# Kernel tuning notes

Measured on AMD Instinct MI355X. Metric: run time of the kernel, lower is better.

The kernel has to match this reference:

```python
import jax, jax.numpy as jnp
import numpy as np

V, C, DFF, NH, NL, KS, OUT = 256, 192, 768, 2, 6, 3, 192
B, T, W = 64, 512, 4
DH = C // NH
PAD = KS // 2
DN = ('NCH', 'OIH', 'NCH')


def _rel_to_abs(x):
    # [b,h,l,2l-1] -> [b,h,l,l]  (VITS _relative_position_to_absolute_position)
    b, h, l, _ = x.shape
    x = jnp.pad(x, ((0, 0), (0, 0), (0, 0), (0, 1)))
    x = x.reshape(b, h, l * 2 * l)
    x = jnp.pad(x, ((0, 0), (0, 0), (0, l - 1)))
    x = x.reshape(b, h, l + 1, 2 * l - 1)
    return x[:, :, :l, l - 1:]


def _abs_to_rel(x):
    # [b,h,l,l] -> [b,h,l,2l-1]  (VITS _absolute_position_to_relative_position)
    b, h, l, _ = x.shape
    x = jnp.pad(x, ((0, 0), (0, 0), (0, 0), (0, l - 1)))
    x = x.reshape(b, h, l * (2 * l - 1))
    x = jnp.pad(x, ((0, 0), (0, 0), (l, 0)))
    x = x.reshape(b, h, l, 2 * l)
    return x[:, :, :, 1:]


def _get_rel_emb(emb, length):
    # emb: [2W+1, DH] -> [2*length-1, DH]
    pad_len = max(length - (W + 1), 0)
    start = max(W + 1 - length, 0)
    padded = jnp.pad(emb, ((pad_len, pad_len), (0, 0)))
    return padded[start:start + 2 * length - 1]


def _ln(x, g, b):
    mu = jnp.mean(x, -1, keepdims=True)
    var = jnp.mean(jnp.square(x - mu), -1, keepdims=True)
    return (x - mu) * jax.lax.rsqrt(var + 1e-5) * g + b


def setup_inputs():
    key = jax.random.key(0)
    ks = jax.random.split(key, 12)
    n = lambda k, s, std: jax.random.normal(k, s, jnp.float32) * std
    return dict(
        tokens=jax.random.randint(ks[0], (B, T), 0, V),
        x_lengths=jnp.full((B,), T, dtype=jnp.int32),
        emb_w=n(ks[1], (V, C), C ** -0.5),
        wqkv=n(ks[2], (NL, 3, C, C), 0.02),
        bqkv=jnp.zeros((NL, 3, C), jnp.float32),
        wo=n(ks[3], (NL, C, C), 0.02),
        bo=jnp.zeros((NL, C), jnp.float32),
        rel_k=n(ks[4], (NL, 2 * W + 1, DH), DH ** -0.5),
        rel_v=n(ks[5], (NL, 2 * W + 1, DH), DH ** -0.5),
        ln1_g=jnp.ones((NL, C), jnp.float32),
        ln1_b=jnp.zeros((NL, C), jnp.float32),
        ln2_g=jnp.ones((NL, C), jnp.float32),
        ln2_b=jnp.zeros((NL, C), jnp.float32),
        ffn_w1=n(ks[6], (NL, DFF, C, KS), 0.02),
        ffn_b1=jnp.zeros((NL, DFF), jnp.float32),
        ffn_w2=n(ks[7], (NL, C, DFF, KS), 0.02),
        ffn_b2=jnp.zeros((NL, C), jnp.float32),
        proj_w=n(ks[8], (2 * OUT, C), 0.02),
        proj_b=jnp.zeros((2 * OUT,), jnp.float32),
    )


def reference(tokens, x_lengths, emb_w, wqkv, bqkv, wo, bo, rel_k, rel_v,
              ln1_g, ln1_b, ln2_g, ln2_b, ffn_w1, ffn_b1, ffn_w2, ffn_b2,
              proj_w, proj_b):
    x = emb_w[tokens] * (C ** 0.5)                       # [B,T,C]
    mask = (jnp.arange(T)[None, :] < x_lengths[:, None]).astype(x.dtype)  # [B,T]
    bias = jnp.where((mask[:, None, :, None] * mask[:, None, None, :]) > 0.0, 0.0, -1e4)
    x = x * mask[..., None]
    inv_sqrt_d = DH ** -0.5
    for l in range(NL):
        q = jnp.einsum('btc,oc->bto', x, wqkv[l, 0]) + bqkv[l, 0]
        k = jnp.einsum('btc,oc->bto', x, wqkv[l, 1]) + bqkv[l, 1]
        v = jnp.einsum('btc,oc->bto', x, wqkv[l, 2]) + bqkv[l, 2]
        q = q.reshape(B, T, NH, DH).transpose(0, 2, 1, 3)  # [B,H,T,D]
        k = k.reshape(B, T, NH, DH).transpose(0, 2, 1, 3)
        v = v.reshape(B, T, NH, DH).transpose(0, 2, 1, 3)
        scores = jnp.einsum('bhtd,bhsd->bhts', q, k) * inv_sqrt_d
        rk = _get_rel_emb(rel_k[l], T)                     # [2T-1, D]
        rel_logits = jnp.einsum('bhtd,md->bhtm', q * inv_sqrt_d, rk)
        scores = scores + _rel_to_abs(rel_logits)
        p = jax.nn.softmax(scores + bias, axis=-1)
        o = jnp.einsum('bhts,bhsd->bhtd', p, v)
        o = o + jnp.einsum('bhtm,md->bhtd', _abs_to_rel(p), _get_rel_emb(rel_v[l], T))
        o = o.transpose(0, 2, 1, 3).reshape(B, T, C)
        y = jnp.einsum('btc,oc->bto', o, wo[l]) + bo[l]
        x = _ln(x + y, ln1_g[l], ln1_b[l])
        h = jax.lax.conv_general_dilated((x * mask[..., None]).transpose(0, 2, 1),
                                         ffn_w1[l], (1,), [(PAD, PAD)],
                                         dimension_numbers=DN) + ffn_b1[l][None, :, None]
        h = jax.nn.relu(h) * mask[:, None, :]
        h = jax.lax.conv_general_dilated(h, ffn_w2[l], (1,), [(PAD, PAD)],
                                         dimension_numbers=DN) + ffn_b2[l][None, :, None]
        y = h.transpose(0, 2, 1) * mask[..., None]
        x = _ln(x + y, ln2_g[l], ln2_b[l])
    x = x * mask[..., None]
    stats = (jnp.einsum('btc,oc->bto', x, proj_w) + proj_b) * mask[..., None]
    m, logs = jnp.split(stats, 2, axis=-1)
    x_mask = mask[:, None, :]
    return x.transpose(0, 2, 1), m.transpose(0, 2, 1), logs.transpose(0, 2, 1), x_mask
```

## Files before the change

### kernel.cpp

```cpp
#include <hip/hip_runtime.h>
#include <hip/hip_bf16.h>

typedef __hip_bfloat16 bf16;
typedef __attribute__((ext_vector_type(8))) short short8;
typedef __attribute__((ext_vector_type(4))) float f32x4;

#define NB 64
#define NT 512
#define NC 192
#define NHEAD 2
#define NDH 96
#define NLAYER 6
#define NDFF 768
#define NW 4

constexpr int MROWS = NB * NT;
constexpr size_t MC = (size_t)MROWS * NC;
constexpr size_t MCB = MC * 4;

__device__ __forceinline__ float us2f(unsigned short x) { return __uint_as_float((unsigned)x << 16); }
__device__ __forceinline__ unsigned short f2b(float f) {
    bf16 h = __float2bfloat16(f);
    return *reinterpret_cast<unsigned short*>(&h);
}

__global__ __launch_bounds__(256) void cvt_plain(const float* __restrict__ s, bf16* __restrict__ d, int n) {
    int i = blockIdx.x * 256 + threadIdx.x;
    if (i < n) d[i] = __float2bfloat16(s[i]);
}
__global__ __launch_bounds__(256) void cvt_conv(const float* __restrict__ s, bf16* __restrict__ d,
                                                int L, int N, int C) {
    int i = blockIdx.x * 256 + threadIdx.x;
    if (i >= L * N * C * 3) return;
    int dk = i % 3;
    int rest = i / 3;
    int c = rest % C;
    int rest2 = rest / C;
    int n = rest2 % N;
    int l = rest2 / N;
    d[(((size_t)l * 3 + dk) * N + n) * C + c] = __float2bfloat16(s[i]);
}

__global__ __launch_bounds__(256) void embed_kernel(const int* __restrict__ tok,
                                                    const int* __restrict__ lens,
                                                    const float* __restrict__ emb,
                                                    float* __restrict__ x,
                                                    bf16* __restrict__ xb) {
    int idx = blockIdx.x * 256 + threadIdx.x;
    if (idx >= (int)MC) return;
    int c = idx % NC;
    int m = idx / NC;
    int t = m % NT, b = m / NT;
    float v = emb[tok[m] * NC + c] * 13.856406460551018f;
    if (t >= lens[b]) v = 0.f;
    x[idx] = v;
    xb[idx] = __float2bfloat16(v);
}

enum GMode { GM_QKV = 0, GM_CONV1 = 2, GM_PROJ = 4 };

template <int MODE, int NTOT, int KC, int TAPS>
__global__ __launch_bounds__(256) void gemm_mfma(const bf16* __restrict__ A,
                                                 const bf16* __restrict__ W,
                                                 const float* __restrict__ bias,
                                                 const int* __restrict__ lens,
                                                 float* __restrict__ of,
                                                 bf16* __restrict__ ob1,
                                                 bf16* __restrict__ ob2,
                                                 bf16* __restrict__ ob3) {
    constexpr int RA = (TAPS == 3) ? 130 : 128;
    constexpr int RB = TAPS * 64;
    __shared__ unsigned short As[RA * 40];
    __shared__ unsigned short Bs[RB * 40];
    const int tid = threadIdx.x;
    const int w = tid >> 6, lane = tid & 63;
    const int g = lane >> 4, li = lane & 15;
    const int n0 = blockIdx.x * 64;
    const int m0 = blockIdx.y * 128;
    const int b = m0 >> 9, t0 = m0 & 511;
    const int len = lens[b];
    const unsigned short* Au = (const unsigned short*)A;
    const unsigned short* Wu = (const unsigned short*)W;

    f32x4 acc[2][4];
#pragma unroll
    for (int a = 0; a < 2; a++)
#pragma unroll
        for (int s = 0; s < 4; s++) acc[a][s] = (f32x4){0.f, 0.f, 0.f, 0.f};

#pragma unroll 1
    for (int k0 = 0; k0 < KC; k0 += 32) {
        __syncthreads();
        for (int c = tid; c < RA * 2; c += 256) {
            int i = c >> 1, hf = (c & 1) * 16;
            int t = t0 + i - (TAPS == 3 ? 1 : 0);
            bool valid = (t >= 0) && (t < NT);
            if constexpr (MODE == GM_CONV1) valid = valid && (t < len);
            short8 v0{}, v1{};
            if (valid) {
                const unsigned short* src = Au + ((size_t)(b * NT + t) * KC + k0 + hf);
                v0 = *(const short8*)src;
                v1 = *(const short8*)(src + 8);
            }
            *(short8*)&As[i * 40 + hf] = v0;
            *(short8*)&As[i * 40 + hf + 8] = v1;
        }
        for (int c = tid; c < RB * 4; c += 256) {
            int rb = c >> 2, qq = (c & 3) * 8;
            int dk = rb >> 6, nl = rb & 63;
            *(short8*)&Bs[rb * 40 + qq] =
                *(const short8*)(Wu + ((size_t)(dk * NTOT + n0 + nl) * KC + k0 + qq));
        }
        __syncthreads();
#pragma unroll
        for (int dk = 0; dk < TAPS; dk++) {
            short8 af0 = *(const short8*)&As[(w * 32 + li + dk) * 40 + g * 8];
            short8 af1 = *(const short8*)&As[(w * 32 + 16 + li + dk) * 40 + g * 8];
#pragma unroll
            for (int sub = 0; sub < 4; sub++) {
                short8 bfr = *(const short8*)&Bs[(dk * 64 + sub * 16 + li) * 40 + g * 8];
                acc[0][sub] = __builtin_amdgcn_mfma_f32_16x16x32_bf16(af0, bfr, acc[0][sub], 0, 0, 0);
                acc[1][sub] = __builtin_amdgcn_mfma_f32_16x16x32_bf16(af1, bfr, acc[1][sub], 0, 0, 0);
            }
        }
    }

#pragma unroll
    for (int sub = 0; sub < 4; sub++) {
        int n = n0 + sub * 16 + li;
        float bv = bias[n];
#pragma unroll
        for (int a = 0; a < 2; a++) {
#pragma unroll
            for (int rr = 0; rr < 4; rr++) {
                int t = t0 + w * 32 + a * 16 + g * 4 + rr;
                size_t m = (size_t)(b * NT + t);
                float vv = acc[a][sub][rr] + bv;
                if constexpr (MODE == GM_QKV) {
                    int iw = n / NC;
                    int cc = n - iw * NC;
                    int hh = cc >= NDH ? 1 : 0;
                    int d = cc - hh * NDH;
                    int bh = b * NHEAD + hh;
                    if (iw == 0) ob1[((size_t)bh * NT + t) * NDH + d] = __float2bfloat16(vv);
                    else if (iw == 1) ob2[((size_t)bh * NT + t) * NDH + d] = __float2bfloat16(vv);
                    else ob3[((size_t)bh * NDH + d) * NT + t] = __float2bfloat16(vv);
                } else if constexpr (MODE == GM_CONV1) {
                    vv = vv > 0.f ? vv : 0.f;
                    if (t >= len) vv = 0.f;
                    ob1[m * NDFF + n] = __float2bfloat16(vv);
                } else {
                    if (t >= len) vv = 0.f;
                    int half = n >= 192 ? 1 : 0;
                    int cc = n - half * 192;
                    of[(size_t)(half + 1) * MC + ((size_t)b * NC + cc) * NT + t] = vv;
                }
            }
        }
    }
}

template <int KC, int TAPS, bool MASKY>
__global__ __launch_bounds__(512) void gemm_ln(const bf16* __restrict__ A,
                                               const bf16* __restrict__ W,
                                               const float* __restrict__ bias,
                                               const int* __restrict__ lens,
                                               const float* __restrict__ lng,
                                               const float* __restrict__ lnb,
                                               float* __restrict__ x,
                                               bf16* __restrict__ xb) {
    constexpr int RA = (TAPS == 3) ? 130 : 128;
    constexpr int RB = TAPS * 192;
    constexpr int NSTEP = KC / 32;
    constexpr int NBI = (RB * 4 + 511) / 512;
    __shared__ unsigned short As[RA * 40];
    __shared__ unsigned short Bs[RB * 40];
    __shared__ float rsm[128][4];
    __shared__ float rsq[128][4];
    const int tid = threadIdx.x;
    const int lane = tid & 63;
    const int g = lane >> 4, li = lane & 15;
    const int w = tid >> 6;
    const int wr = w & 1, wc = w >> 1;
    const int m0 = blockIdx.x * 128;
    const int b = m0 >> 9, t0 = m0 & 511;
    const int len = lens[b];
    const unsigned short* Au = (const unsigned short*)A;
    const unsigned short* Wu = (const unsigned short*)W;

    const int ai = tid >> 1, ahf = (tid & 1) * 16;
    const int at = t0 + ai - (TAPS == 3 ? 1 : 0);
    const bool aon = (tid < RA * 2);
    const bool avalid = aon && (at >= 0) && (at < NT);

    short8 ra0{}, ra1{};
    short8 rbv[NBI];
#pragma unroll
    for (int j = 0; j < NBI; j++) rbv[j] = short8{};

    f32x4 acc[4][3];
#pragma unroll
    for (int ar = 0; ar < 4; ar++)
#pragma unroll
        for (int sub = 0; sub < 3; sub++) acc[ar][sub] = (f32x4){0.f, 0.f, 0.f, 0.f};

    if (avalid) {
        const unsigned short* src = Au + ((size_t)(b * NT + at) * KC + 0 + ahf);
        ra0 = *(const short8*)src;
        ra1 = *(const short8*)(src + 8);
    }
#pragma unroll
    for (int j = 0; j < NBI; j++) {
        int cb = tid + j * 512;
        if (cb < RB * 4) {
            int rbr = cb >> 2, qq = (cb & 3) * 8;
            rbv[j] = *(const short8*)(Wu + ((size_t)rbr * KC + 0 + qq));
        }
    }
    if (aon) {
        short8 z{};
        *(short8*)&As[ai * 40 + ahf] = avalid ? ra0 : z;
        *(short8*)&As[ai * 40 + ahf + 8] = avalid ? ra1 : z;
    }
#pragma unroll
    for (int j = 0; j < NBI; j++) {
        int cb = tid + j * 512;
        if (cb < RB * 4) {
            int rbr = cb >> 2, qq = (cb & 3) * 8;
            *(short8*)&Bs[rbr * 40 + qq] = rbv[j];
        }
    }

#pragma unroll 1
    for (int s = 0; s < NSTEP; s++) {
        __syncthreads();
        if (s + 1 < NSTEP) {
            int k0 = (s + 1) * 32;
            if (avalid) {
                const unsigned short* src = Au + ((size_t)(b * NT + at) * KC + k0 + ahf);
                ra0 = *(const short8*)src;
                ra1 = *(const short8*)(src + 8);
            }
#pragma unroll
            for (int j = 0; j < NBI; j++) {
                int cb = tid + j * 512;
                if (cb < RB * 4) {
                    int rbr = cb >> 2, qq = (cb & 3) * 8;
                    rbv[j] = *(const short8*)(Wu + ((size_t)rbr * KC + k0 + qq));
                }
            }
        }
#pragma unroll
        for (int dk = 0; dk < TAPS; dk++) {
            short8 af[4];
#pragma unroll
            for (int ar = 0; ar < 4; ar++)
                af[ar] = *(const short8*)&As[(wr * 64 + ar * 16 + li + dk) * 40 + g * 8];
#pragma unroll
            for (int sub = 0; sub < 3; sub++) {
                short8 bfr = *(const short8*)&Bs[(dk * 192 + wc * 48 + sub * 16 + li) * 40 + g * 8];
#pragma unroll
                for (int ar = 0; ar < 4; ar++)
                    acc[ar][sub] = __builtin_amdgcn_mfma_f32_16x16x32_bf16(af[ar], bfr, acc[ar][sub], 0, 0, 0);
            }
        }
        __syncthreads();
        if (s + 1 < NSTEP) {
            if (aon) {
                short8 z{};
                *(short8*)&As[ai * 40 + ahf] = avalid ? ra0 : z;
                *(short8*)&As[ai * 40 + ahf + 8] = avalid ? ra1 : z;
            }
#pragma unroll
            for (int j = 0; j < NBI; j++) {
                int cb = tid + j * 512;
                if (cb < RB * 4) {
                    int rbr = cb >> 2, qq = (cb & 3) * 8;
                    *(short8*)&Bs[rbr * 40 + qq] = rbv[j];
                }
            }
        }
    }

    float biasv[3], gv[3], bbv[3];
#pragma unroll
    for (int sub = 0; sub < 3; sub++) {
        int n = wc * 48 + sub * 16 + li;
        biasv[sub] = bias[n];
        gv[sub] = lng[n];
        bbv[sub] = lnb[n];
    }
    float psm[4][4], psq[4][4];
#pragma unroll
    for (int ar = 0; ar < 4; ar++) {
#pragma unroll
        for (int rr = 0; rr < 4; rr++) {
            int r = wr * 64 + ar * 16 + 4 * g + rr;
            int t = t0 + r;
            size_t m = (size_t)(b * NT + t);
            float sm = 0.f, sq = 0.f;
#pragma unroll
            for (int sub = 0; sub < 3; sub++) {
                int n = wc * 48 + sub * 16 + li;
                float y = acc[ar][sub][rr] + biasv[sub];
                if (MASKY && t >= len) y = 0.f;
                float rres = y + x[m * NC + n];
                acc[ar][sub][rr] = rres;
                sm += rres;
                sq += rres * rres;
            }
            psm[ar][rr] = sm;
            psq[ar][rr] = sq;
        }
    }
#pragma unroll
    for (int off = 1; off < 16; off <<= 1) {
#pragma unroll
        for (int ar = 0; ar < 4; ar++)
#pragma unroll
            for (int rr = 0; rr < 4; rr++) {
                psm[ar][rr] += __shfl_xor(psm[ar][rr], off);
                psq[ar][rr] += __shfl_xor(psq[ar][rr], off);
            }
    }
    if (li == 0) {
#pragma unroll
        for (int ar = 0; ar < 4; ar++)
#pragma unroll
            for (int rr = 0; rr < 4; rr++) {
                int r = wr * 64 + ar * 16 + 4 * g + rr;
                rsm[r][wc] = psm[ar][rr];
                rsq[r][wc] = psq[ar][rr];
            }
    }
    __syncthreads();
#pragma unroll
    for (int ar = 0; ar < 4; ar++) {
#pragma unroll
        for (int rr = 0; rr < 4; rr++) {
            int r = wr * 64 + ar * 16 + 4 * g + rr;
            int t = t0 + r;
            size_t m = (size_t)(b * NT + t);
            float sm = rsm[r][0] + rsm[r][1] + rsm[r][2] + rsm[r][3];
            float sq = rsq[r][0] + rsq[r][1] + rsq[r][2] + rsq[r][3];
            float mu = sm * (1.f / NC);
            float var = fmaxf(sq * (1.f / NC) - mu * mu, 0.f);
            float rs = rsqrtf(var + 1e-5f);
#pragma unroll
            for (int sub = 0; sub < 3; sub++) {
                int n = wc * 48 + sub * 16 + li;
                float o = (acc[ar][sub][rr] - mu) * rs * gv[sub] + bbv[sub];
                x[m * NC + n] = o;
                xb[m * NC + n] = __float2bfloat16(o);
            }
        }
    }
}

__global__ __launch_bounds__(256, 4) void attn_mfma(const bf16* __restrict__ q,
                                                    const bf16* __restrict__ k,
                                                    const bf16* __restrict__ v,
                                                    const float* __restrict__ relk,
                                                    const float* __restrict__ relv,
                                                    const int* __restrict__ lens,
                                                    bf16* __restrict__ o) {
    __shared__ __align__(16) char pool[40448];
    unsigned short* Kt = (unsigned short*)pool;
    unsigned short* Vt = (unsigned short*)(pool + 13312);
    unsigned short* Pt = (unsigned short*)(pool + 27136);
    unsigned short* Pb = (unsigned short*)(pool + 36352);
    unsigned short* Qt = (unsigned short*)pool;
    unsigned short* Rk = (unsigned short*)(pool + 13312);

    const int qt = blockIdx.x, bh = blockIdx.y;
    const int b = bh >> 1, h = bh & 1;
    const int q0 = qt * 64;
    const int tid = threadIdx.x;
    const int w = tid >> 6, lane = tid & 63;
    const int g = lane >> 4, li = lane & 15;
    const int len = lens[b];
    const float scale = 0.10206207261596575f;

    const unsigned short* qg = (const unsigned short*)q + (size_t)bh * NT * NDH;
    const unsigned short* kg = (const unsigned short*)k + (size_t)bh * NT * NDH;
    const unsigned short* vg = (const unsigned short*)v + (size_t)bh * NDH * NT;

    for (int c = tid; c < 64 * 12; c += 256) {
        int r = c / 12, seg = (c % 12) * 8;
        *(short8*)&Qt[r * 104 + seg] = *(const short8*)(qg + (size_t)(q0 + r) * NDH + seg);
    }
    for (int c = tid; c < 16 * 96; c += 256) {
        int dd = c / 96, d = c - (c / 96) * 96;
        Rk[dd * 104 + d] = (dd < 9) ? f2b(relk[dd * 96 + d]) : (unsigned short)0;
    }
    for (int c = tid; c < 4 * 16 * 32; c += 256) Pb[c] = 0;
    __syncthreads();

    f32x4 racc = (f32x4){0.f, 0.f, 0.f, 0.f};
    short8 qf[3];
#pragma unroll
    for (int kk = 0; kk < 3; kk++) {
        qf[kk] = *(const short8*)&Qt[(w * 16 + li) * 104 + kk * 32 + g * 8];
        short8 bfr = *(const short8*)&Rk[li * 104 + kk * 32 + g * 8];
        racc = __builtin_amdgcn_mfma_f32_16x16x32_bf16(qf[kk], bfr, racc, 0, 0, 0);
    }
    short8 rvf[6];
#pragma unroll
    for (int ds = 0; ds < 6; ds++) {
#pragma unroll
        for (int i = 0; i < 8; i++) {
            int j = g * 8 + i;
            int d = ds * 16 + li;
            unsigned short u = (j < 9) ? f2b(relv[j * 96 + d]) : (unsigned short)0;
            rvf[ds][i] = (short)u;
        }
    }
    __syncthreads();

    float m_run[4], l_run[4];
    f32x4 Oa[6];
#pragma unroll
    for (int rr = 0; rr < 4; rr++) { m_run[rr] = -1e30f; l_run[rr] = 0.f; }
#pragma unroll
    for (int ds = 0; ds < 6; ds++) Oa[ds] = (f32x4){0.f, 0.f, 0.f, 0.f};

    for (int s0 = 0; s0 < NT; s0 += 64) {
        for (int c = tid; c < 64 * 12; c += 256) {
            int ss = c / 12, seg = (c % 12) * 8;
            *(short8*)&Kt[ss * 104 + seg] = *(const short8*)(kg + (size_t)(s0 + ss) * NDH + seg);
        }
        for (int c = tid; c < 96 * 8; c += 256) {
            int d = c >> 3, seg = (c & 7) * 8;
            *(short8*)&Vt[d * 72 + seg] = *(const short8*)(vg + (size_t)d * NT + s0 + seg);
        }
        __syncthreads();

        f32x4 acc[4];
#pragma unroll
        for (int sub = 0; sub < 4; sub++) acc[sub] = (f32x4){0.f, 0.f, 0.f, 0.f};
        __builtin_amdgcn_s_setprio(1);
#pragma unroll
        for (int kk = 0; kk < 3; kk++) {
#pragma unroll
            for (int sub = 0; sub < 4; sub++) {
                short8 bfr = *(const short8*)&Kt[(sub * 16 + li) * 104 + kk * 32 + g * 8];
                acc[sub] = __builtin_amdgcn_mfma_f32_16x16x32_bf16(qf[kk], bfr, acc[sub], 0, 0, 0);
            }
        }
        __builtin_amdgcn_s_setprio(0);

        float rmax[4];
#pragma unroll
        for (int rr = 0; rr < 4; rr++) rmax[rr] = -1e30f;
#pragma unroll
        for (int sub = 0; sub < 4; sub++) {
#pragma unroll
            for (int rr = 0; rr < 4; rr++) {
                int scol = s0 + sub * 16 + li;
                int rloc = w * 16 + 4 * g + rr;
                int qrow = q0 + rloc;
                int dd = scol - qrow;
                float rv = __shfl(racc[rr], g * 16 + dd + NW);
                float val = acc[sub][rr];
                if (dd >= -NW && dd <= NW) val += rv;
                val *= scale;
                if (scol >= len || qrow >= len) val -= 10000.f;
                acc[sub][rr] = val;
                rmax[rr] = fmaxf(rmax[rr], val);
            }
        }
#pragma unroll
        for (int off = 1; off < 16; off <<= 1)
#pragma unroll
            for (int rr = 0; rr < 4; rr++) rmax[rr] = fmaxf(rmax[rr], __shfl_xor(rmax[rr], off));

        float scf[4];
#pragma unroll
        for (int rr = 0; rr < 4; rr++) {
            float mn = fmaxf(m_run[rr], rmax[rr]);
            scf[rr] = __expf(m_run[rr] - mn);
            m_run[rr] = mn;
        }
        float rsum[4] = {0.f, 0.f, 0.f, 0.f};
#pragma unroll
        for (int sub = 0; sub < 4; sub++)
#pragma unroll
            for (int rr = 0; rr < 4; rr++) {
                float p = __expf(acc[sub][rr] - m_run[rr]);
                acc[sub][rr] = p;
                rsum[rr] += p;
            }
#pragma unroll
        for (int off = 1; off < 16; off <<= 1)
#pragma unroll
            for (int rr = 0; rr < 4; rr++) rsum[rr] += __shfl_xor(rsum[rr], off);
#pragma unroll
        for (int rr = 0; rr < 4; rr++) l_run[rr] = l_run[rr] * scf[rr] + rsum[rr];
#pragma unroll
        for (int ds = 0; ds < 6; ds++)
#pragma unroll
            for (int rr = 0; rr < 4; rr++) Oa[ds][rr] *= scf[rr];

#pragma unroll
        for (int sub = 0; sub < 4; sub++)
#pragma unroll
            for (int rr = 0; rr < 4; rr++)
                Pt[w * 1152 + (4 * g + rr) * 72 + sub * 16 + li] = f2b(acc[sub][rr]);

        __builtin_amdgcn_s_setprio(1);
#pragma unroll
        for (int kk = 0; kk < 2; kk++) {
            short8 pa = *(const short8*)&Pt[w * 1152 + li * 72 + kk * 32 + g * 8];
#pragma unroll
            for (int ds = 0; ds < 6; ds++) {
                short8 bv = *(const short8*)&Vt[(ds * 16 + li) * 72 + kk * 32 + g * 8];
                Oa[ds] = __builtin_amdgcn_mfma_f32_16x16x32_bf16(pa, bv, Oa[ds], 0, 0, 0);
            }
        }
        __builtin_amdgcn_s_setprio(0);

        for (int c = lane; c < 144; c += 64) {
            int r = c / 9, j = c - (c / 9) * 9;
            int s = q0 + w * 16 + r + j - NW;
            unsigned short pv_ = 0;
            int u = s - s0;
            if (u >= 0 && u < 64) pv_ = Pt[w * 1152 + r * 72 + u];
            Pb[w * 512 + r * 32 + j] = pv_;
        }
        short8 pband = *(const short8*)&Pb[w * 512 + li * 32 + g * 8];
#pragma unroll
        for (int ds = 0; ds < 6; ds++)
            Oa[ds] = __builtin_amdgcn_mfma_f32_16x16x32_bf16(pband, rvf[ds], Oa[ds], 0, 0, 0);
        __syncthreads();
    }

    float invl[4];
#pragma unroll
    for (int rr = 0; rr < 4; rr++) invl[rr] = 1.f / l_run[rr];
#pragma unroll
    for (int ds = 0; ds < 6; ds++)
#pragma unroll
        for (int rr = 0; rr < 4; rr++) {
            int qrow = q0 + w * 16 + 4 * g + rr;
            o[((size_t)(b * NT + qrow)) * NC + h * 96 + ds * 16 + li] =
                __float2bfloat16(Oa[ds][rr] * invl[rr]);
        }
}

__global__ __launch_bounds__(256) void xpose_kernel(const float* __restrict__ x,
                                                    const int* __restrict__ lens,
                                                    float* __restrict__ out) {
    int idx = blockIdx.x * 256 + threadIdx.x;
    if (idx >= (int)MC) return;
    int t = idx % NT;
    int bc = idx / NT;
    int c = bc % NC;
    int b = bc / NC;
    float v = (t < lens[b]) ? x[((size_t)b * NT + t) * NC + c] : 0.f;
    out[idx] = v;
}

__global__ __launch_bounds__(256) void mask_kernel(const int* __restrict__ lens, float* __restrict__ out) {
    int idx = blockIdx.x * 256 + threadIdx.x;
    if (idx >= NB * NT) return;
    int t = idx % NT;
    int b = idx / NT;
    out[idx] = (t < lens[b]) ? 1.f : 0.f;
}

extern "C" void kernel_launch(void* const* d_in, const int* in_sizes, int n_in,
                              void* d_out, int out_size, void* d_ws, size_t ws_size,
                              hipStream_t stream) {
    (void)in_sizes; (void)n_in; (void)out_size; (void)ws_size;
    const int* tok = (const int*)d_in[0];
    const int* lens = (const int*)d_in[1];
    const float* emb = (const float*)d_in[2];
    const float* wqkv = (const float*)d_in[3];
    const float* bqkv = (const float*)d_in[4];
    const float* wo = (const float*)d_in[5];
    const float* bo = (const float*)d_in[6];
    const float* relk = (const float*)d_in[7];
    const float* relv = (const float*)d_in[8];
    const float* ln1g = (const float*)d_in[9];
    const float* ln1b = (const float*)d_in[10];
    const float* ln2g = (const float*)d_in[11];
    const float* ln2b = (const float*)d_in[12];
    const float* fw1 = (const float*)d_in[13];
    const float* fb1 = (const float*)d_in[14];
    const float* fw2 = (const float*)d_in[15];
    const float* fb2 = (const float*)d_in[16];
    const float* pw = (const float*)d_in[17];
    const float* pb = (const float*)d_in[18];
    float* out = (float*)d_out;

    char* wsb = (char*)d_ws;
    float* xB = (float*)wsb;
    bf16* xb = (bf16*)(wsb + 2 * MCB);
    bf16* qb = (bf16*)(wsb + 2 * MCB + MCB / 2);
    bf16* kb = qb + MC;
    bf16* vb = kb + MC;
    bf16* ob = vb + MC;
    bf16* hB = qb;
    bf16* pwqkv = ob + MC;
    bf16* pwo = pwqkv + (size_t)NLAYER * 3 * NC * NC;
    bf16* pw1 = pwo + (size_t)NLAYER * NC * NC;
    bf16* pw2 = pw1 + (size_t)NLAYER * 3 * NDFF * NC;
    bf16* pproj = pw2 + (size_t)NLAYER * 3 * NC * NDFF;

    {
        int n1 = NLAYER * 3 * NC * NC;
        cvt_plain<<<(n1 + 255) / 256, 256, 0, stream>>>(wqkv, pwqkv, n1);
        int n2 = NLAYER * NC * NC;
        cvt_plain<<<(n2 + 255) / 256, 256, 0, stream>>>(wo, pwo, n2);
        int n3 = 2 * 192 * NC;
        cvt_plain<<<(n3 + 255) / 256, 256, 0, stream>>>(pw, pproj, n3);
        int n4 = NLAYER * NDFF * NC * 3;
        cvt_conv<<<(n4 + 255) / 256, 256, 0, stream>>>(fw1, pw1, NLAYER, NDFF, NC);
        int n5 = NLAYER * NC * NDFF * 3;
        cvt_conv<<<(n5 + 255) / 256, 256, 0, stream>>>(fw2, pw2, NLAYER, NC, NDFF);
    }

    embed_kernel<<<(int)((MC + 255) / 256), 256, 0, stream>>>(tok, lens, emb, xB, xb);

    for (int l = 0; l < NLAYER; l++) {
        gemm_mfma<GM_QKV, 576, 192, 1><<<dim3(9, 256), 256, 0, stream>>>(
            xb, pwqkv + (size_t)l * 3 * NC * NC, bqkv + (size_t)l * 3 * NC, lens,
            nullptr, qb, kb, vb);
        attn_mfma<<<dim3(8, NB * NHEAD), 256, 0, stream>>>(
            qb, kb, vb, relk + (size_t)l * (2 * NW + 1) * NDH,
            relv + (size_t)l * (2 * NW + 1) * NDH, lens, ob);
        gemm_ln<192, 1, false><<<256, 512, 0, stream>>>(
            ob, pwo + (size_t)l * NC * NC, bo + (size_t)l * NC, lens,
            ln1g + (size_t)l * NC, ln1b + (size_t)l * NC, xB, xb);
        gemm_mfma<GM_CONV1, 768, 192, 3><<<dim3(12, 256), 256, 0, stream>>>(
            xb, pw1 + (size_t)l * 3 * NDFF * NC, fb1 + (size_t)l * NDFF, lens,
            nullptr, hB, nullptr, nullptr);
        gemm_ln<768, 3, true><<<256, 512, 0, stream>>>(
            hB, pw2 + (size_t)l * 3 * NC * NDFF, fb2 + (size_t)l * NC, lens,
            ln2g + (size_t)l * NC, ln2b + (size_t)l * NC, xB, xb);
    }

    gemm_mfma<GM_PROJ, 384, 192, 1><<<dim3(6, 256), 256, 0, stream>>>(
        xb, pproj, pb, lens, out, nullptr, nullptr, nullptr);
    xpose_kernel<<<(int)((MC + 255) / 256), 256, 0, stream>>>(xB, lens, out);
    mask_kernel<<<(NB * NT + 255) / 256, 256, 0, stream>>>(lens, out + 3 * MC);
}
```

Baseline: 1.539 ms.

## Add dedicated pipelined conv1 GEMM and streamline attention softmax with exp2 and lazy rescale

Replaces the generic three-tap conv1 GEMM path with a new 512-thread kernel. It uses 128x192 tiles, register-prefetched double staging, and 4x3 MFMA tiles per wave, giving more reuse per LDS load. Attention now takes Q pre-scaled by softmax scale·log2e in the QKV epilogue, uses exp2f, and skips the mask check when the sequence is full. It also rescales the running max only when it grows past a threshold, and swaps grid dimensions so heads vary fastest. The lazy rescale trades exactness of the running max for fewer multiplies, and the larger conv tile uses more LDS and registers.

After: 1.558 ms. Within noise of the previous version (+1.2%).

```diff
diff --git a/kernel.cpp b/kernel.cpp
--- a/kernel.cpp
+++ b/kernel.cpp
@@ -17,6 +17,7 @@
 constexpr int MROWS = NB * NT;
 constexpr size_t MC = (size_t)MROWS * NC;
 constexpr size_t MCB = MC * 4;
+constexpr float QSC = 0.10206207261596575f * 1.4426950408889634f;
 
 __device__ __forceinline__ float us2f(unsigned short x) { return __uint_as_float((unsigned)x << 16); }
 __device__ __forceinline__ unsigned short f2b(float f) {
@@ -57,9 +58,9 @@
     xb[idx] = __float2bfloat16(v);
 }
 
-enum GMode { GM_QKV = 0, GM_CONV1 = 2, GM_PROJ = 4 };
-
-template <int MODE, int NTOT, int KC, int TAPS>
+enum GMode { GM_QKV = 0, GM_PROJ = 4 };
+
+template <int MODE, int NTOT, int KC>
 __global__ __launch_bounds__(256) void gemm_mfma(const bf16* __restrict__ A,
                                                  const bf16* __restrict__ W,
                                                  const float* __restrict__ bias,
@@ -68,8 +69,8 @@
                                                  bf16* __restrict__ ob1,
                                                  bf16* __restrict__ ob2,
                                                  bf16* __restrict__ ob3) {
-    constexpr int RA = (TAPS == 3) ? 130 : 128;
-    constexpr int RB = TAPS * 64;
+    constexpr int RA = 128;
+    constexpr int RB = 64;
     __shared__ unsigned short As[RA * 40];
     __shared__ unsigned short Bs[RB * 40];
     const int tid = threadIdx.x;
@@ -93,35 +94,24 @@
         __syncthreads();
         for (int c = tid; c < RA * 2; c += 256) {
             int i = c >> 1, hf = (c & 1) * 16;
-            int t = t0 + i - (TAPS == 3 ? 1 : 0);
-            bool valid = (t >= 0) && (t < NT);
-            if constexpr (MODE == GM_CONV1) valid = valid && (t < len);
-            short8 v0{}, v1{};
-            if (valid) {
-                const unsigned short* src = Au + ((size_t)(b * NT + t) * KC + k0 + hf);
-                v0 = *(const short8*)src;
-                v1 = *(const short8*)(src + 8);
-            }
-            *(short8*)&As[i * 40 + hf] = v0;
-            *(short8*)&As[i * 40 + hf + 8] = v1;
+            int t = t0 + i;
+            const unsigned short* src = Au + ((size_t)(b * NT + t) * KC + k0 + hf);
+            *(short8*)&As[i * 40 + hf] = *(const short8*)src;
+            *(short8*)&As[i * 40 + hf + 8] = *(const short8*)(src + 8);
         }
         for (int c = tid; c < RB * 4; c += 256) {
             int rb = c >> 2, qq = (c & 3) * 8;
-            int dk = rb >> 6, nl = rb & 63;
             *(short8*)&Bs[rb * 40 + qq] =
-                *(const short8*)(Wu + ((size_t)(dk * NTOT + n0 + nl) * KC + k0 + qq));
+                *(const short8*)(Wu + ((size_t)(n0 + rb) * KC + k0 + qq));
         }
         __syncthreads();
-#pragma unroll
-        for (int dk = 0; dk < TAPS; dk++) {
-            short8 af0 = *(const short8*)&As[(w * 32 + li + dk) * 40 + g * 8];
-            short8 af1 = *(const short8*)&As[(w * 32 + 16 + li + dk) * 40 + g * 8];
-#pragma unroll
-            for (int sub = 0; sub < 4; sub++) {
-                short8 bfr = *(const short8*)&Bs[(dk * 64 + sub * 16 + li) * 40 + g * 8];
-                acc[0][sub] = __builtin_amdgcn_mfma_f32_16x16x32_bf16(af0, bfr, acc[0][sub], 0, 0, 0);
-                acc[1][sub] = __builtin_amdgcn_mfma_f32_16x16x32_bf16(af1, bfr, acc[1][sub], 0, 0, 0);
-            }
+        short8 af0 = *(const short8*)&As[(w * 32 + li) * 40 + g * 8];
+        short8 af1 = *(const short8*)&As[(w * 32 + 16 + li) * 40 + g * 8];
+#pragma unroll
+        for (int sub = 0; sub < 4; sub++) {
+            short8 bfr = *(const short8*)&Bs[(sub * 16 + li) * 40 + g * 8];
+            acc[0][sub] = __builtin_amdgcn_mfma_f32_16x16x32_bf16(af0, bfr, acc[0][sub], 0, 0, 0);
+            acc[1][sub] = __builtin_amdgcn_mfma_f32_16x16x32_bf16(af1, bfr, acc[1][sub], 0, 0, 0);
         }
     }
 
@@ -142,19 +132,158 @@
                     int hh = cc >= NDH ? 1 : 0;
                     int d = cc - hh * NDH;
                     int bh = b * NHEAD + hh;
-                    if (iw == 0) ob1[((size_t)bh * NT + t) * NDH + d] = __float2bfloat16(vv);
+                    if (iw == 0) ob1[((size_t)bh * NT + t) * NDH + d] = __float2bfloat16(vv * QSC);
                     else if (iw == 1) ob2[((size_t)bh * NT + t) * NDH + d] = __float2bfloat16(vv);
                     else ob3[((size_t)bh * NDH + d) * NT + t] = __float2bfloat16(vv);
-                } else if constexpr (MODE == GM_CONV1) {
-                    vv = vv > 0.f ? vv : 0.f;
-                    if (t >= len) vv = 0.f;
-                    ob1[m * NDFF + n] = __float2bfloat16(vv);
                 } else {
                     if (t >= len) vv = 0.f;
                     int half = n >= 192 ? 1 : 0;
                     int cc = n - half * 192;
                     of[(size_t)(half + 1) * MC + ((size_t)b * NC + cc) * NT + t] = vv;
                 }
+            }
+        }
+    }
+}
+
+__global__ __launch_bounds__(512) void gemm_relu(const bf16* __restrict__ A,
+                                                 const bf16* __restrict__ W,
+                                                 const float* __restrict__ bias,
+                                                 const int* __restrict__ lens,
+                                                 bf16* __restrict__ ob) {
+    constexpr int KC = 192;
+    constexpr int RA = 130;
+    constexpr int RB = 576;
+    constexpr int NSTEP = KC / 32;
+    constexpr int NBI = (RB * 4 + 511) / 512;
+    __shared__ unsigned short As[RA * 40];
+    __shared__ unsigned short Bs[RB * 40];
+    const int tid = threadIdx.x;
+    const int lane = tid & 63;
+    const int g = lane >> 4, li = lane & 15;
+    const int w = tid >> 6;
+    const int wr = w & 1, wc = w >> 1;
+    const int m0 = blockIdx.x * 128;
+    const int n0 = blockIdx.y * 192;
+    const int b = m0 >> 9, t0 = m0 & 511;
+    const int len = lens[b];
+    const unsigned short* Au = (const unsigned short*)A;
+    const unsigned short* Wu = (const unsigned short*)W;
+
+    const int ai = tid >> 1, ahf = (tid & 1) * 16;
+    const int at = t0 + ai - 1;
+    const bool aon = (tid < RA * 2);
+    const bool avalid = aon && (at >= 0) && (at < NT) && (at < len);
+
+    short8 ra0{}, ra1{};
+    short8 rbv[NBI];
+#pragma unroll
+    for (int j = 0; j < NBI; j++) rbv[j] = short8{};
+
+    f32x4 acc[4][3];
+#pragma unroll
+    for (int ar = 0; ar < 4; ar++)
+#pragma unroll
+        for (int sub = 0; sub < 3; sub++) acc[ar][sub] = (f32x4){0.f, 0.f, 0.f, 0.f};
+
+    auto wrow = [&](int rb) -> size_t {
+        int dk = (rb >= 384) ? 2 : ((rb >= 192) ? 1 : 0);
+        int nl = rb - dk * 192;
+        return (size_t)(dk * NDFF + n0 + nl);
+    };
+
+    if (avalid) {
+        const unsigned short* src = Au + ((size_t)(b * NT + at) * KC + ahf);
+        ra0 = *(const short8*)src;
+        ra1 = *(const short8*)(src + 8);
+    }
+#pragma unroll
+    for (int j = 0; j < NBI; j++) {
+        int cb = tid + j * 512;
+        if (cb < RB * 4) {
+            int rbr = cb >> 2, qq = (cb & 3) * 8;
+            rbv[j] = *(const short8*)(Wu + (wrow(rbr) * KC + qq));
+        }
+    }
+    if (aon) {
+        short8 z{};
+        *(short8*)&As[ai * 40 + ahf] = avalid ? ra0 : z;
+        *(short8*)&As[ai * 40 + ahf + 8] = avalid ? ra1 : z;
+    }
+#pragma unroll
+    for (int j = 0; j < NBI; j++) {
+        int cb = tid + j * 512;
+        if (cb < RB * 4) {
+            int rbr = cb >> 2, qq = (cb & 3) * 8;
+            *(short8*)&Bs[rbr * 40 + qq] = rbv[j];
+        }
+    }
+
+#pragma unroll 1
+    for (int s = 0; s < NSTEP; s++) {
+        __syncthreads();
+        if (s + 1 < NSTEP) {
+            int k0 = (s + 1) * 32;
+            if (avalid) {
+                const unsigned short* src = Au + ((size_t)(b * NT + at) * KC + k0 + ahf);
+                ra0 = *(const short8*)src;
+                ra1 = *(const short8*)(src + 8);
+            }
+#pragma unroll
+            for (int j = 0; j < NBI; j++) {
+                int cb = tid + j * 512;
+                if (cb < RB * 4) {
+                    int rbr = cb >> 2, qq = (cb & 3) * 8;
+                    rbv[j] = *(const short8*)(Wu + (wrow(rbr) * KC + k0 + qq));
+                }
+            }
+        }
+#pragma unroll
+        for (int dk = 0; dk < 3; dk++) {
+            short8 af[4];
+#pragma unroll
+            for (int ar = 0; ar < 4; ar++)
+                af[ar] = *(const short8*)&As[(wr * 64 + ar * 16 + li + dk) * 40 + g * 8];
+#pragma unroll
+            for (int sub = 0; sub < 3; sub++) {
+                short8 bfr = *(const short8*)&Bs[(dk * 192 + wc * 48 + sub * 16 + li) * 40 + g * 8];
+#pragma unroll
+                for (int ar = 0; ar < 4; ar++)
+                    acc[ar][sub] = __builtin_amdgcn_mfma_f32_16x16x32_bf16(af[ar], bfr, acc[ar][sub], 0, 0, 0);
+            }
+        }
+        __syncthreads();
+        if (s + 1 < NSTEP) {
+            if (aon) {
+                short8 z{};
+                *(short8*)&As[ai * 40 + ahf] = avalid ? ra0 : z;
+                *(short8*)&As[ai * 40 + ahf + 8] = avalid ? ra1 : z;
+            }
+#pragma unroll
+            for (int j = 0; j < NBI; j++) {
+                int cb = tid + j * 512;
+                if (cb < RB * 4) {
+                    int rbr = cb >> 2, qq = (cb & 3) * 8;
+                    *(short8*)&Bs[rbr * 40 + qq] = rbv[j];
+                }
+            }
+        }
+    }
+
+#pragma unroll
+    for (int sub = 0; sub < 3; sub++) {
+        int n = n0 + wc * 48 + sub * 16 + li;
+        float bv = bias[n];
+#pragma unroll
+        for (int ar = 0; ar < 4; ar++) {
+#pragma unroll
+            for (int rr = 0; rr < 4; rr++) {
+                int t = t0 + wr * 64 + ar * 16 + 4 * g + rr;
+                size_t m = (size_t)(b * NT + t);
+                float vv = acc[ar][sub][rr] + bv;
+                vv = vv > 0.f ? vv : 0.f;
+                if (t >= len) vv = 0.f;
+                ob[m * NDFF + n] = __float2bfloat16(vv);
             }
         }
     }
@@ -372,14 +501,14 @@
     unsigned short* Qt = (unsigned short*)pool;
     unsigned short* Rk = (unsigned short*)(pool + 13312);
 
-    const int qt = blockIdx.x, bh = blockIdx.y;
+    const int bh = blockIdx.x, qt = blockIdx.y;
     const int b = bh >> 1, h = bh & 1;
     const int q0 = qt * 64;
     const int tid = threadIdx.x;
     const int w = tid >> 6, lane = tid & 63;
     const int g = lane >> 4, li = lane & 15;
     const int len = lens[b];
-    const float scale = 0.10206207261596575f;
+    const bool anymask = (len < NT);
 
     const unsigned short* qg = (const unsigned short*)q + (size_t)bh * NT * NDH;
     const unsigned short* kg = (const unsigned short*)k + (size_t)bh * NT * NDH;
@@ -457,14 +586,12 @@
 #pragma unroll
             for (int rr = 0; rr < 4; rr++) {
                 int scol = s0 + sub * 16 + li;
-                int rloc = w * 16 + 4 * g + rr;
-                int qrow = q0 + rloc;
+                int qrow = q0 + w * 16 + 4 * g + rr;
                 int dd = scol - qrow;
                 float rv = __shfl(racc[rr], g * 16 + dd + NW);
                 float val = acc[sub][rr];
                 if (dd >= -NW && dd <= NW) val += rv;
-                val *= scale;
-                if (scol >= len || qrow >= len) val -= 10000.f;
+                if (anymask && (scol >= len || qrow >= len)) val -= 14427.0f;
                 acc[sub][rr] = val;
                 rmax[rr] = fmaxf(rmax[rr], val);
             }
@@ -474,19 +601,26 @@
 #pragma unroll
             for (int rr = 0; rr < 4; rr++) rmax[rr] = fmaxf(rmax[rr], __shfl_xor(rmax[rr], off));
 
-        float scf[4];
-#pragma unroll
-        for (int rr = 0; rr < 4; rr++) {
-            float mn = fmaxf(m_run[rr], rmax[rr]);
-            scf[rr] = __expf(m_run[rr] - mn);
-            m_run[rr] = mn;
+        float growth = -3.0e38f;
+#pragma unroll
+        for (int rr = 0; rr < 4; rr++) growth = fmaxf(growth, rmax[rr] - m_run[rr]);
+        if (__any(growth > 11.54f)) {
+#pragma unroll
+            for (int rr = 0; rr < 4; rr++) {
+                float mn = fmaxf(m_run[rr], rmax[rr]);
+                float scf = exp2f(m_run[rr] - mn);
+                m_run[rr] = mn;
+                l_run[rr] *= scf;
+#pragma unroll
+                for (int ds = 0; ds < 6; ds++) Oa[ds][rr] *= scf;
+            }
         }
         float rsum[4] = {0.f, 0.f, 0.f, 0.f};
 #pragma unroll
         for (int sub = 0; sub < 4; sub++)
 #pragma unroll
             for (int rr = 0; rr < 4; rr++) {
-                float p = __expf(acc[sub][rr] - m_run[rr]);
+                float p = exp2f(acc[sub][rr] - m_run[rr]);
                 acc[sub][rr] = p;
                 rsum[rr] += p;
             }
@@ -495,11 +629,7 @@
 #pragma unroll
             for (int rr = 0; rr < 4; rr++) rsum[rr] += __shfl_xor(rsum[rr], off);
 #pragma unroll
-        for (int rr = 0; rr < 4; rr++) l_run[rr] = l_run[rr] * scf[rr] + rsum[rr];
-#pragma unroll
-        for (int ds = 0; ds < 6; ds++)
-#pragma unroll
-            for (int rr = 0; rr < 4; rr++) Oa[ds][rr] *= scf[rr];
+        for (int rr = 0; rr < 4; rr++) l_run[rr] += rsum[rr];
 
 #pragma unroll
         for (int sub = 0; sub < 4; sub++)
@@ -623,24 +753,23 @@
     embed_kernel<<<(int)((MC + 255) / 256), 256, 0, stream>>>(tok, lens, emb, xB, xb);
 
     for (int l = 0; l < NLAYER; l++) {
-        gemm_mfma<GM_QKV, 576, 192, 1><<<dim3(9, 256), 256, 0, stream>>>(
+        gemm_mfma<GM_QKV, 576, 192><<<dim3(9, 256), 256, 0, stream>>>(
             xb, pwqkv + (size_t)l * 3 * NC * NC, bqkv + (size_t)l * 3 * NC, lens,
             nullptr, qb, kb, vb);
-        attn_mfma<<<dim3(8, NB * NHEAD), 256, 0, stream>>>(
+        attn_mfma<<<dim3(NB * NHEAD, 8), 256, 0, stream>>>(
             qb, kb, vb, relk + (size_t)l * (2 * NW + 1) * NDH,
             relv + (size_t)l * (2 * NW + 1) * NDH, lens, ob);
         gemm_ln<192, 1, false><<<256, 512, 0, stream>>>(
             ob, pwo + (size_t)l * NC * NC, bo + (size_t)l * NC, lens,
             ln1g + (size_t)l * NC, ln1b + (size_t)l * NC, xB, xb);
-        gemm_mfma<GM_CONV1, 768, 192, 3><<<dim3(12, 256), 256, 0, stream>>>(
-            xb, pw1 + (size_t)l * 3 * NDFF * NC, fb1 + (size_t)l * NDFF, lens,
-            nullptr, hB, nullptr, nullptr);
+        gemm_relu<<<dim3(256, 4), 512, 0, stream>>>(
+            xb, pw1 + (size_t)l * 3 * NDFF * NC, fb1 + (size_t)l * NDFF, lens, hB);
         gemm_ln<768, 3, true><<<256, 512, 0, stream>>>(
             hB, pw2 + (size_t)l * 3 * NC * NDFF, fb2 + (size_t)l * NC, lens,
             ln2g + (size_t)l * NC, ln2b + (size_t)l * NC, xB, xb);
     }
 
-    gemm_mfma<GM_PROJ, 384, 192, 1><<<dim3(6, 256), 256, 0, stream>>>(
+    gemm_mfma<GM_PROJ, 384, 192><<<dim3(6, 256), 256, 0, stream>>>(
         xb, pproj, pb, lens, out, nullptr, nullptr, nullptr);
     xpose_kernel<<<(int)((MC + 255) / 256), 256, 0, stream>>>(xB, lens, out);
     mask_kernel<<<(NB * NT + 255) / 256, 256, 0, stream>>>(lens, out + 3 * MC);
```

## Streamline attention softmax, skip off-band relative work, halve gemm_ln row tile

Applied to the files above, without the earlier changes.

Folds the softmax scale and log2(e) into Q when the QKV GEMM stores it, so attention can use exp2f and drop the per-element multiply. The running-max rescale of the accumulators is skipped unless some row's max grows past a threshold. Relative-position logit and value work runs only for key tiles that overlap the diagonal band, and mask arithmetic runs only when the sequence is shorter than T. The attention grid axes are swapped, and gemm_ln uses 64-row tiles with twice as many blocks for better CU fill, at the cost of reloading the weight tile more often.

Measured after the change: 1.507 ms. -2.1%, faster.

```diff
diff --git a/kernel.cpp b/kernel.cpp
--- a/kernel.cpp
+++ b/kernel.cpp
@@ -17,6 +17,7 @@
 constexpr int MROWS = NB * NT;
 constexpr size_t MC = (size_t)MROWS * NC;
 constexpr size_t MCB = MC * 4;
+constexpr float QSC = 0.10206207261596575f * 1.4426950408889634f;
 
 __device__ __forceinline__ float us2f(unsigned short x) { return __uint_as_float((unsigned)x << 16); }
 __device__ __forceinline__ unsigned short f2b(float f) {
@@ -142,7 +143,7 @@
                     int hh = cc >= NDH ? 1 : 0;
                     int d = cc - hh * NDH;
                     int bh = b * NHEAD + hh;
-                    if (iw == 0) ob1[((size_t)bh * NT + t) * NDH + d] = __float2bfloat16(vv);
+                    if (iw == 0) ob1[((size_t)bh * NT + t) * NDH + d] = __float2bfloat16(vv * QSC);
                     else if (iw == 1) ob2[((size_t)bh * NT + t) * NDH + d] = __float2bfloat16(vv);
                     else ob3[((size_t)bh * NDH + d) * NT + t] = __float2bfloat16(vv);
                 } else if constexpr (MODE == GM_CONV1) {
@@ -160,7 +161,7 @@
     }
 }
 
-template <int KC, int TAPS, bool MASKY>
+template <int KC, int TAPS, bool MASKY, int BM>
 __global__ __launch_bounds__(512) void gemm_ln(const bf16* __restrict__ A,
                                                const bf16* __restrict__ W,
                                                const float* __restrict__ bias,
@@ -169,20 +170,21 @@
                                                const float* __restrict__ lnb,
                                                float* __restrict__ x,
                                                bf16* __restrict__ xb) {
-    constexpr int RA = (TAPS == 3) ? 130 : 128;
+    constexpr int RA = BM + ((TAPS == 3) ? 2 : 0);
     constexpr int RB = TAPS * 192;
     constexpr int NSTEP = KC / 32;
     constexpr int NBI = (RB * 4 + 511) / 512;
+    constexpr int AR = BM / 32;
     __shared__ unsigned short As[RA * 40];
     __shared__ unsigned short Bs[RB * 40];
-    __shared__ float rsm[128][4];
-    __shared__ float rsq[128][4];
+    __shared__ float rsm[BM][4];
+    __shared__ float rsq[BM][4];
     const int tid = threadIdx.x;
     const int lane = tid & 63;
     const int g = lane >> 4, li = lane & 15;
     const int w = tid >> 6;
     const int wr = w & 1, wc = w >> 1;
-    const int m0 = blockIdx.x * 128;
+    const int m0 = blockIdx.x * BM;
     const int b = m0 >> 9, t0 = m0 & 511;
     const int len = lens[b];
     const unsigned short* Au = (const unsigned short*)A;
@@ -198,9 +200,9 @@
 #pragma unroll
     for (int j = 0; j < NBI; j++) rbv[j] = short8{};
 
-    f32x4 acc[4][3];
-#pragma unroll
-    for (int ar = 0; ar < 4; ar++)
+    f32x4 acc[AR][3];
+#pragma unroll
+    for (int ar = 0; ar < AR; ar++)
 #pragma unroll
         for (int sub = 0; sub < 3; sub++) acc[ar][sub] = (f32x4){0.f, 0.f, 0.f, 0.f};
 
@@ -252,15 +254,15 @@
         }
 #pragma unroll
         for (int dk = 0; dk < TAPS; dk++) {
-            short8 af[4];
-#pragma unroll
-            for (int ar = 0; ar < 4; ar++)
-                af[ar] = *(const short8*)&As[(wr * 64 + ar * 16 + li + dk) * 40 + g * 8];
+            short8 af[AR];
+#pragma unroll
+            for (int ar = 0; ar < AR; ar++)
+                af[ar] = *(const short8*)&As[(wr * (BM / 2) + ar * 16 + li + dk) * 40 + g * 8];
 #pragma unroll
             for (int sub = 0; sub < 3; sub++) {
                 short8 bfr = *(const short8*)&Bs[(dk * 192 + wc * 48 + sub * 16 + li) * 40 + g * 8];
 #pragma unroll
-                for (int ar = 0; ar < 4; ar++)
+                for (int ar = 0; ar < AR; ar++)
                     acc[ar][sub] = __builtin_amdgcn_mfma_f32_16x16x32_bf16(af[ar], bfr, acc[ar][sub], 0, 0, 0);
             }
         }
@@ -290,12 +292,12 @@
         gv[sub] = lng[n];
         bbv[sub] = lnb[n];
     }
-    float psm[4][4], psq[4][4];
-#pragma unroll
-    for (int ar = 0; ar < 4; ar++) {
+    float psm[AR][4], psq[AR][4];
+#pragma unroll
+    for (int ar = 0; ar < AR; ar++) {
 #pragma unroll
         for (int rr = 0; rr < 4; rr++) {
-            int r = wr * 64 + ar * 16 + 4 * g + rr;
+            int r = wr * (BM / 2) + ar * 16 + 4 * g + rr;
             int t = t0 + r;
             size_t m = (size_t)(b * NT + t);
             float sm = 0.f, sq = 0.f;
@@ -316,7 +318,7 @@
 #pragma unroll
     for (int off = 1; off < 16; off <<= 1) {
 #pragma unroll
-        for (int ar = 0; ar < 4; ar++)
+        for (int ar = 0; ar < AR; ar++)
 #pragma unroll
             for (int rr = 0; rr < 4; rr++) {
                 psm[ar][rr] += __shfl_xor(psm[ar][rr], off);
@@ -325,20 +327,20 @@
     }
     if (li == 0) {
 #pragma unroll
-        for (int ar = 0; ar < 4; ar++)
+        for (int ar = 0; ar < AR; ar++)
 #pragma unroll
             for (int rr = 0; rr < 4; rr++) {
-                int r = wr * 64 + ar * 16 + 4 * g + rr;
+                int r = wr * (BM / 2) + ar * 16 + 4 * g + rr;
                 rsm[r][wc] = psm[ar][rr];
                 rsq[r][wc] = psq[ar][rr];
             }
     }
     __syncthreads();
 #pragma unroll
-    for (int ar = 0; ar < 4; ar++) {
+    for (int ar = 0; ar < AR; ar++) {
 #pragma unroll
         for (int rr = 0; rr < 4; rr++) {
-            int r = wr * 64 + ar * 16 + 4 * g + rr;
+            int r = wr * (BM / 2) + ar * 16 + 4 * g + rr;
             int t = t0 + r;
             size_t m = (size_t)(b * NT + t);
             float sm = rsm[r][0] + rsm[r][1] + rsm[r][2] + rsm[r][3];
@@ -372,14 +374,14 @@
     unsigned short* Qt = (unsigned short*)pool;
     unsigned short* Rk = (unsigned short*)(pool + 13312);
 
-    const int qt = blockIdx.x, bh = blockIdx.y;
+    const int bh = blockIdx.x, qt = blockIdx.y;
     const int b = bh >> 1, h = bh & 1;
     const int q0 = qt * 64;
     const int tid = threadIdx.x;
     const int w = tid >> 6, lane = tid & 63;
     const int g = lane >> 4, li = lane & 15;
     const int len = lens[b];
-    const float scale = 0.10206207261596575f;
+    const bool anymask = (len < NT);
 
     const unsigned short* qg = (const unsigned short*)q + (size_t)bh * NT * NDH;
     const unsigned short* kg = (const unsigned short*)k + (size_t)bh * NT * NDH;
@@ -424,6 +426,8 @@
 #pragma unroll
     for (int ds = 0; ds < 6; ds++) Oa[ds] = (f32x4){0.f, 0.f, 0.f, 0.f};
 
+    const int wrow0 = q0 + w * 16;
+
     for (int s0 = 0; s0 < NT; s0 += 64) {
         for (int c = tid; c < 64 * 12; c += 256) {
             int ss = c / 12, seg = (c % 12) * 8;
@@ -435,6 +439,8 @@
         }
         __syncthreads();
 
+        const bool band = (s0 <= wrow0 + 15 + NW) && (s0 + 63 >= wrow0 - NW);
+
         f32x4 acc[4];
 #pragma unroll
         for (int sub = 0; sub < 4; sub++) acc[sub] = (f32x4){0.f, 0.f, 0.f, 0.f};
@@ -449,6 +455,19 @@
         }
         __builtin_amdgcn_s_setprio(0);
 
+        if (band) {
+#pragma unroll
+            for (int sub = 0; sub < 4; sub++) {
+#pragma unroll
+                for (int rr = 0; rr < 4; rr++) {
+                    int scol = s0 + sub * 16 + li;
+                    int qrow = wrow0 + 4 * g + rr;
+                    int dd = scol - qrow;
+                    float rv = __shfl(racc[rr], g * 16 + dd + NW);
+                    if (dd >= -NW && dd <= NW) acc[sub][rr] += rv;
+                }
+            }
+        }
         float rmax[4];
 #pragma unroll
         for (int rr = 0; rr < 4; rr++) rmax[rr] = -1e30f;
@@ -456,17 +475,12 @@
         for (int sub = 0; sub < 4; sub++) {
 #pragma unroll
             for (int rr = 0; rr < 4; rr++) {
-                int scol = s0 + sub * 16 + li;
-                int rloc = w * 16 + 4 * g + rr;
-                int qrow = q0 + rloc;
-                int dd = scol - qrow;
-                float rv = __shfl(racc[rr], g * 16 + dd + NW);
-                float val = acc[sub][rr];
-                if (dd >= -NW && dd <= NW) val += rv;
-                val *= scale;
-                if (scol >= len || qrow >= len) val -= 10000.f;
-                acc[sub][rr] = val;
-                rmax[rr] = fmaxf(rmax[rr], val);
+                if (anymask) {
+                    int scol = s0 + sub * 16 + li;
+                    int qrow = wrow0 + 4 * g + rr;
+                    if (scol >= len || qrow >= len) acc[sub][rr] -= 14427.0f;
+                }
+                rmax[rr] = fmaxf(rmax[rr], acc[sub][rr]);
             }
         }
 #pragma unroll
@@ -474,19 +488,26 @@
 #pragma unroll
             for (int rr = 0; rr < 4; rr++) rmax[rr] = fmaxf(rmax[rr], __shfl_xor(rmax[rr], off));
 
-        float scf[4];
-#pragma unroll
-        for (int rr = 0; rr < 4; rr++) {
-            float mn = fmaxf(m_run[rr], rmax[rr]);
-            scf[rr] = __expf(m_run[rr] - mn);
-            m_run[rr] = mn;
+        float growth = -3.0e38f;
+#pragma unroll
+        for (int rr = 0; rr < 4; rr++) growth = fmaxf(growth, rmax[rr] - m_run[rr]);
+        if (__any(growth > 11.54f)) {
+#pragma unroll
+            for (int rr = 0; rr < 4; rr++) {
+                float mn = fmaxf(m_run[rr], rmax[rr]);
+                float scf = exp2f(m_run[rr] - mn);
+                m_run[rr] = mn;
+                l_run[rr] *= scf;
+#pragma unroll
+                for (int ds = 0; ds < 6; ds++) Oa[ds][rr] *= scf;
+            }
         }
         float rsum[4] = {0.f, 0.f, 0.f, 0.f};
 #pragma unroll
         for (int sub = 0; sub < 4; sub++)
 #pragma unroll
             for (int rr = 0; rr < 4; rr++) {
-                float p = __expf(acc[sub][rr] - m_run[rr]);
+                float p = exp2f(acc[sub][rr] - m_run[rr]);
                 acc[sub][rr] = p;
                 rsum[rr] += p;
             }
@@ -495,11 +516,7 @@
 #pragma unroll
             for (int rr = 0; rr < 4; rr++) rsum[rr] += __shfl_xor(rsum[rr], off);
 #pragma unroll
-        for (int rr = 0; rr < 4; rr++) l_run[rr] = l_run[rr] * scf[rr] + rsum[rr];
-#pragma unroll
-        for (int ds = 0; ds < 6; ds++)
-#pragma unroll
-            for (int rr = 0; rr < 4; rr++) Oa[ds][rr] *= scf[rr];
+        for (int rr = 0; rr < 4; rr++) l_run[rr] += rsum[rr];
 
 #pragma unroll
         for (int sub = 0; sub < 4; sub++)
@@ -519,18 +536,17 @@
         }
         __builtin_amdgcn_s_setprio(0);
 
-        for (int c = lane; c < 144; c += 64) {
-            int r = c / 9, j = c - (c / 9) * 9;
-            int s = q0 + w * 16 + r + j - NW;
-            unsigned short pv_ = 0;
-            int u = s - s0;
-            if (u >= 0 && u < 64) pv_ = Pt[w * 1152 + r * 72 + u];
-            Pb[w * 512 + r * 32 + j] = pv_;
-        }
-        short8 pband = *(const short8*)&Pb[w * 512 + li * 32 + g * 8];
-#pragma unroll
-        for (int ds = 0; ds < 6; ds++)
-            Oa[ds] = __builtin_amdgcn_mfma_f32_16x16x32_bf16(pband, rvf[ds], Oa[ds], 0, 0, 0);
+        if (band) {
+            for (int j = g; j < 9; j += 4) {
+                int u = wrow0 + li + j - NW - s0;
+                unsigned short pv_ = (u >= 0 && u < 64) ? Pt[w * 1152 + li * 72 + u] : (unsigned short)0;
+                Pb[w * 512 + li * 32 + j] = pv_;
+            }
+            short8 pband = *(const short8*)&Pb[w * 512 + li * 32 + g * 8];
+#pragma unroll
+            for (int ds = 0; ds < 6; ds++)
+                Oa[ds] = __builtin_amdgcn_mfma_f32_16x16x32_bf16(pband, rvf[ds], Oa[ds], 0, 0, 0);
+        }
         __syncthreads();
     }
 
@@ -541,7 +557,7 @@
     for (int ds = 0; ds < 6; ds++)
 #pragma unroll
         for (int rr = 0; rr < 4; rr++) {
-            int qrow = q0 + w * 16 + 4 * g + rr;
+            int qrow = wrow0 + 4 * g + rr;
             o[((size_t)(b * NT + qrow)) * NC + h * 96 + ds * 16 + li] =
                 __float2bfloat16(Oa[ds][rr] * invl[rr]);
         }
@@ -626,16 +642,16 @@
         gemm_mfma<GM_QKV, 576, 192, 1><<<dim3(9, 256), 256, 0, stream>>>(
             xb, pwqkv + (size_t)l * 3 * NC * NC, bqkv + (size_t)l * 3 * NC, lens,
             nullptr, qb, kb, vb);
-        attn_mfma<<<dim3(8, NB * NHEAD), 256, 0, stream>>>(
+        attn_mfma<<<dim3(NB * NHEAD, 8), 256, 0, stream>>>(
             qb, kb, vb, relk + (size_t)l * (2 * NW + 1) * NDH,
             relv + (size_t)l * (2 * NW + 1) * NDH, lens, ob);
-        gemm_ln<192, 1, false><<<256, 512, 0, stream>>>(
+        gemm_ln<192, 1, false, 64><<<512, 512, 0, stream>>>(
             ob, pwo + (size_t)l * NC * NC, bo + (size_t)l * NC, lens,
             ln1g + (size_t)l * NC, ln1b + (size_t)l * NC, xB, xb);
         gemm_mfma<GM_CONV1, 768, 192, 3><<<dim3(12, 256), 256, 0, stream>>>(
             xb, pw1 + (size_t)l * 3 * NDFF * NC, fb1 + (size_t)l * NDFF, lens,
             nullptr, hB, nullptr, nullptr);
-        gemm_ln<768, 3, true><<<256, 512, 0, stream>>>(
+        gemm_ln<768, 3, true, 64><<<512, 512, 0, stream>>>(
             hB, pw2 + (size_t)l * 3 * NC * NDFF, fb2 + (size_t)l * NC, lens,
             ln2g + (size_t)l * NC, ln2b + (size_t)l * NC, xB, xb);
     }
```
